# Performance work log

Measured on AMD Instinct MI355X. Metric: run time of the kernel, lower is better.

Reference implementation:

```python
import jax, jax.numpy as jnp
import numpy as np

B, D, H = 4096, 1024, 1024
LN_EPS = 1e-5


def setup_inputs() -> dict:
    key = jax.random.key(0)
    ks = jax.random.split(key, 5)
    return {
        "x": jax.random.normal(ks[0], (B, D), dtype=jnp.float32),
        "prev_h": jax.random.normal(ks[1], (B, H), dtype=jnp.float32),
        "prev_c": jax.random.normal(ks[2], (B, H), dtype=jnp.float32),
        "Wx": jax.random.normal(ks[3], (D, 4 * H), dtype=jnp.float32) * 0.01,
        "Wh": jax.random.normal(ks[4], (H, 4 * H), dtype=jnp.float32) * 0.01,
        "b": jnp.zeros((4 * H,), dtype=jnp.float32),
        "ln_gamma": jnp.ones((4 * H,), dtype=jnp.float32),
        "ln_beta": jnp.zeros((4 * H,), dtype=jnp.float32),
    }


def reference(x, prev_h, prev_c, Wx, Wh, b, ln_gamma, ln_beta):
    # pre-activations: [B, 4H]
    a = x @ Wx + prev_h @ Wh + b
    # LayerNorm over last dim (use_ln=True)
    mu = jnp.mean(a, axis=-1, keepdims=True)
    var = jnp.mean(jnp.square(a - mu), axis=-1, keepdims=True)
    a = (a - mu) * jax.lax.rsqrt(var + LN_EPS) * ln_gamma + ln_beta
    i = jax.nn.sigmoid(a[:, :H])
    f = jax.nn.sigmoid(a[:, H:2 * H])
    o = jax.nn.sigmoid(a[:, 2 * H:3 * H])
    g = jnp.tanh(a[:, 3 * H:])
    next_c = f * prev_c + i * g
    next_h = o * jnp.tanh(next_c)
    # dropout=0.0 -> identity
    return (next_h, next_c)
```

## Files before the change

### kernel.cpp

```cpp
#include <hip/hip_runtime.h>
#include <hip/hip_bf16.h>
#include <stdint.h>

typedef unsigned short u16;
typedef __attribute__((ext_vector_type(8))) short short8;
typedef __attribute__((ext_vector_type(16))) float f32x16;

#define B_DIM 4096
#define D_DIM 1024
#define H_DIM 1024
#define K_DIM 2048
#define N_DIM 4096
#define LN_EPS 1e-5f

__device__ __forceinline__ u16 f2bf(float f) {
    union { float f; uint32_t u; } v; v.f = f;
    uint32_t u = v.u;
    uint32_t r = (u + 0x7FFFu + ((u >> 16) & 1u)) >> 16;
    return (u16)r;
}
__device__ __forceinline__ float bf2f(u16 h) {
    union { uint32_t u; float f; } v; v.u = ((uint32_t)h) << 16;
    return v.f;
}
__device__ __forceinline__ void gld16(const u16* g, u16* l) {
    __builtin_amdgcn_global_load_lds(
        (const __attribute__((address_space(1))) void*)g,
        (__attribute__((address_space(3))) void*)l,
        16, 0, 0);
}
__device__ __forceinline__ float sigm(float x) { return 1.0f / (1.0f + __expf(-x)); }
__device__ __forceinline__ float tanh_fast(float x) { return 1.0f - 2.0f / (__expf(2.0f * x) + 1.0f); }

__global__ __launch_bounds__(256) void prep(const float* __restrict__ x,
                                            const float* __restrict__ h,
                                            const float* __restrict__ Wx,
                                            const float* __restrict__ Wh,
                                            u16* __restrict__ A,
                                            u16* __restrict__ Bt) {
    __shared__ u16 tile[64 * 64];
    const int t = threadIdx.x;
    if (blockIdx.x < 4096) {
        int id = blockIdx.x * 256 + t;
        int row = id >> 8;
        int col = (id & 255) * 8;
        const float* src = (col < D_DIM) ? (x + (size_t)row * D_DIM + col)
                                         : (h + (size_t)row * H_DIM + (col - D_DIM));
        float4 v0 = ((const float4*)src)[0];
        float4 v1 = ((const float4*)src)[1];
        union { u16 us[8]; uint4 u; } p;
        p.us[0] = f2bf(v0.x); p.us[1] = f2bf(v0.y); p.us[2] = f2bf(v0.z); p.us[3] = f2bf(v0.w);
        p.us[4] = f2bf(v1.x); p.us[5] = f2bf(v1.y); p.us[6] = f2bf(v1.z); p.us[7] = f2bf(v1.w);
        *(uint4*)(A + (size_t)id * 8) = p.u;
    } else {
        const int v = blockIdx.x - 4096;
        const int n0 = (v & 63) * 64;
        const int k0 = (v >> 6) * 64;
        const int kl  = t >> 4;
        const int nl4 = (t & 15) * 4;
#pragma unroll
        for (int it = 0; it < 4; ++it) {
            const int klocal = kl + it * 16;
            const int k = k0 + klocal;
            const float* src = (k < D_DIM) ? (Wx + (size_t)k * N_DIM)
                                           : (Wh + (size_t)(k - D_DIM) * N_DIM);
            float4 w = *(const float4*)(src + n0 + nl4);
            union { u16 us[4]; uint2 u; } p;
            p.us[0] = f2bf(w.x); p.us[1] = f2bf(w.y); p.us[2] = f2bf(w.z); p.us[3] = f2bf(w.w);
            const int swz = 8 * ((klocal >> 4) & 3);
            *(uint2*)(tile + klocal * 64 + (nl4 ^ swz)) = p.u;
        }
        __syncthreads();
        const int nl = t >> 2;
        const int kp = (t & 3) * 16;
        const int swz = 8 * (t & 3);
        union { u16 us[16]; uint4 q[2]; } o;
#pragma unroll
        for (int i = 0; i < 16; ++i)
            o.us[i] = tile[(kp + i) * 64 + (nl ^ swz)];
        u16* dst = Bt + (size_t)(n0 + nl) * K_DIM + k0 + kp;
        *(uint4*)dst = o.q[0];
        *(uint4*)(dst + 8) = o.q[1];
    }
}

__global__ __launch_bounds__(256, 1) void gemm_bf16(const u16* __restrict__ A,
                                                    const u16* __restrict__ Bt,
                                                    const float* __restrict__ bias,
                                                    u16* __restrict__ C) {
    __shared__ u16 As[2][16384];
    __shared__ u16 Bs[2][16384];
    const int tid = threadIdx.x;
    const int wave = tid >> 6, lane = tid & 63;
    const int m0 = blockIdx.y * 256;
    const int n0 = blockIdx.x * 256;
    const int wm = (wave & 1) * 128;
    const int wn = (wave >> 1) * 128;

    f32x16 acc[4][4] = {};

    const int perm = ((lane & 3) - (lane >> 3)) & 3;
    const int vofs = (lane >> 2) * K_DIM + perm * 8;
    const int lr = lane & 31, half = lane >> 5;

    for (int it = 0; it < K_DIM / 64 + 1; ++it) {
        if (it < K_DIM / 64) {
            const int kt = it * 64;
            const int buf = it & 1;
#pragma unroll
            for (int q = 0; q < 8; ++q) {
                const int ch = wave * 8 + q;
                const int hp = ch >> 4, c = ch & 15;
                const int so = (c * 16) * K_DIM + kt + hp * 32;
                const int ldso = hp * 8192 + c * 512;
                gld16(A  + (size_t)m0 * K_DIM + so + vofs, &As[buf][ldso]);
                gld16(Bt + (size_t)n0 * K_DIM + so + vofs, &Bs[buf][ldso]);
            }
        }
        if (it == 0) { __syncthreads(); continue; }

        const int cbuf = (it - 1) & 1;
#pragma unroll
        for (int kk = 0; kk < 4; ++kk) {
            const int hp = kk >> 1;
            const int s = (((kk & 1) * 2 + half) + (lr >> 1)) & 3;
            const int ko = hp * 8192 + s * 8;
            short8 af[4], bf[4];
#pragma unroll
            for (int i = 0; i < 4; ++i)
                af[i] = *(const short8*)(&As[cbuf][ko + (wm + i * 32 + lr) * 32]);
#pragma unroll
            for (int j = 0; j < 4; ++j)
                bf[j] = *(const short8*)(&Bs[cbuf][ko + (wn + j * 32 + lr) * 32]);
#pragma unroll
            for (int i = 0; i < 4; ++i)
#pragma unroll
                for (int j = 0; j < 4; ++j)
                    acc[i][j] = __builtin_amdgcn_mfma_f32_32x32x16_bf16(af[i], bf[j], acc[i][j], 0, 0, 0);
        }
        __syncthreads();
    }

#pragma unroll
    for (int i = 0; i < 4; ++i) {
#pragma unroll
        for (int j = 0; j < 4; ++j) {
            const int c = n0 + wn + 32 * j + lr;
            const float bb = bias[c];
#pragma unroll
            for (int reg = 0; reg < 16; ++reg) {
                const int row = m0 + wm + 32 * i + (reg & 3) + 8 * (reg >> 2) + 4 * half;
                C[(size_t)row * N_DIM + c] = f2bf(acc[i][j][reg] + bb);
            }
        }
    }
}

__global__ __launch_bounds__(256) void ln_lstm(const u16* __restrict__ aT,
                                               const float* __restrict__ pc,
                                               const float* __restrict__ gamma,
                                               const float* __restrict__ beta,
                                               float* __restrict__ out) {
    const int row = blockIdx.x;
    const int t = threadIdx.x;
    const u16* ar = aT + (size_t)row * N_DIM;
    const int j0 = t * 4;

    union U2 { uint2 u; u16 us[4]; };
    U2 g4[4];
#pragma unroll
    for (int s = 0; s < 4; ++s) g4[s].u = *(const uint2*)(ar + s * H_DIM + j0);

    float sum = 0.f, ssq = 0.f;
#pragma unroll
    for (int s = 0; s < 4; ++s)
#pragma unroll
        for (int e = 0; e < 4; ++e) { float v = bf2f(g4[s].us[e]); sum += v; ssq += v * v; }

#pragma unroll
    for (int off = 32; off > 0; off >>= 1) {
        sum += __shfl_down(sum, off, 64);
        ssq += __shfl_down(ssq, off, 64);
    }
    __shared__ float red[8];
    if ((t & 63) == 0) { red[t >> 6] = sum; red[4 + (t >> 6)] = ssq; }
    __syncthreads();
    const float ts = red[0] + red[1] + red[2] + red[3];
    const float tq = red[4] + red[5] + red[6] + red[7];
    const float mu = ts * (1.0f / N_DIM);
    const float var = fmaxf(tq * (1.0f / N_DIM) - mu * mu, 0.0f);
    const float rs = rsqrtf(var + LN_EPS);

    float vi[4], vf[4], vo[4], vg[4];
    auto gate = [&](int s, float* v) {
        const int off = s * H_DIM;
        float4 gm = *(const float4*)(gamma + off + j0);
        float4 bt = *(const float4*)(beta + off + j0);
        v[0] = (bf2f(g4[s].us[0]) - mu) * rs * gm.x + bt.x;
        v[1] = (bf2f(g4[s].us[1]) - mu) * rs * gm.y + bt.y;
        v[2] = (bf2f(g4[s].us[2]) - mu) * rs * gm.z + bt.z;
        v[3] = (bf2f(g4[s].us[3]) - mu) * rs * gm.w + bt.w;
    };
    gate(0, vi); gate(1, vf); gate(2, vo); gate(3, vg);

    float4 c4 = *(const float4*)(pc + (size_t)row * H_DIM + j0);
    float cin[4] = {c4.x, c4.y, c4.z, c4.w};
    float nh[4], nc[4];
#pragma unroll
    for (int r = 0; r < 4; ++r) {
        float ig = sigm(vi[r]);
        float fg = sigm(vf[r]);
        float og = sigm(vo[r]);
        float gg = tanh_fast(vg[r]);
        nc[r] = fg * cin[r] + ig * gg;
        nh[r] = og * tanh_fast(nc[r]);
    }
    float4 h4 = {nh[0], nh[1], nh[2], nh[3]};
    float4 c4o = {nc[0], nc[1], nc[2], nc[3]};
    *(float4*)(out + (size_t)row * H_DIM + j0) = h4;
    *(float4*)(out + (size_t)B_DIM * H_DIM + (size_t)row * H_DIM + j0) = c4o;
}

extern "C" void kernel_launch(void* const* d_in, const int* in_sizes, int n_in,
                              void* d_out, int out_size, void* d_ws, size_t ws_size,
                              hipStream_t stream) {
    const float* x  = (const float*)d_in[0];
    const float* ph = (const float*)d_in[1];
    const float* pc = (const float*)d_in[2];
    const float* Wx = (const float*)d_in[3];
    const float* Wh = (const float*)d_in[4];
    const float* b  = (const float*)d_in[5];
    const float* gm = (const float*)d_in[6];
    const float* bt = (const float*)d_in[7];
    float* out = (float*)d_out;

    char* ws = (char*)d_ws;
    u16* Abf = (u16*)ws;
    u16* Btb = (u16*)(ws + (size_t)16 * 1024 * 1024);
    u16* aT  = (u16*)(ws + (size_t)32 * 1024 * 1024);

    prep<<<dim3(4096 + 2048), dim3(256), 0, stream>>>(x, ph, Wx, Wh, Abf, Btb);
    gemm_bf16<<<dim3(16, 16), dim3(256), 0, stream>>>(Abf, Btb, b, aT);
    ln_lstm<<<dim3(4096), dim3(256), 0, stream>>>(aT, pc, gm, bt, out);
}
```

Baseline: 224.2 us.

## Restructure bf16 GEMM into 8-wave half-K-step pipeline with block swizzle

Doubles the GEMM workgroup to 8 waves, each computing a 128x64 sub-tile, and splits each 64-wide K tile into two 32-wide halves. Global-to-LDS loads of upcoming halves are issued between the LDS fragment reads and the MFMA burst, with explicit vmcnt waits, barriers and setprio raised around the MFMAs. A block-index swizzle also remaps tiles to change L2 locality. The aim is better overlap of memory and MFMA work with less register pressure per wave, at the cost of more barriers and hand-tuned wait counts that must match the issued loads exactly.

```diff
diff --git a/kernel.cpp b/kernel.cpp
--- a/kernel.cpp
+++ b/kernel.cpp
@@ -84,7 +84,7 @@
     }
 }
 
-__global__ __launch_bounds__(256, 1) void gemm_bf16(const u16* __restrict__ A,
+__global__ __launch_bounds__(512, 2) void gemm_bf16(const u16* __restrict__ A,
                                                     const u16* __restrict__ Bt,
                                                     const float* __restrict__ bias,
                                                     u16* __restrict__ C) {
@@ -92,59 +92,93 @@
     __shared__ u16 Bs[2][16384];
     const int tid = threadIdx.x;
     const int wave = tid >> 6, lane = tid & 63;
-    const int m0 = blockIdx.y * 256;
-    const int n0 = blockIdx.x * 256;
+
+    const int bid = blockIdx.y * 16 + blockIdx.x;
+    const int swz_bid = (bid & 7) * 32 + (bid >> 3);
+    const int m0 = (swz_bid >> 4) * 256;
+    const int n0 = (swz_bid & 15) * 256;
+
     const int wm = (wave & 1) * 128;
-    const int wn = (wave >> 1) * 128;
-
-    f32x16 acc[4][4] = {};
+    const int wn = (wave >> 1) * 64;
+
+    f32x16 acc[4][2] = {};
 
     const int perm = ((lane & 3) - (lane >> 3)) & 3;
     const int vofs = (lane >> 2) * K_DIM + perm * 8;
     const int lr = lane & 31, half = lane >> 5;
 
-    for (int it = 0; it < K_DIM / 64 + 1; ++it) {
-        if (it < K_DIM / 64) {
-            const int kt = it * 64;
-            const int buf = it & 1;
-#pragma unroll
-            for (int q = 0; q < 8; ++q) {
-                const int ch = wave * 8 + q;
-                const int hp = ch >> 4, c = ch & 15;
-                const int so = (c * 16) * K_DIM + kt + hp * 32;
-                const int ldso = hp * 8192 + c * 512;
-                gld16(A  + (size_t)m0 * K_DIM + so + vofs, &As[buf][ldso]);
-                gld16(Bt + (size_t)n0 * K_DIM + so + vofs, &Bs[buf][ldso]);
-            }
+    const u16* Ab = A  + (size_t)m0 * K_DIM;
+    const u16* Bb = Bt + (size_t)n0 * K_DIM;
+
+    auto stage = [&](int buf, int t, int h) {
+        const int kt = t * 64;
+#pragma unroll
+        for (int q = 0; q < 2; ++q) {
+            const int c = wave * 2 + q;
+            const int so = (c * 16) * K_DIM + kt + h * 32;
+            const int ldso = h * 8192 + c * 512;
+            gld16(Ab + so + vofs, &As[buf][ldso]);
+            gld16(Bb + so + vofs, &Bs[buf][ldso]);
         }
-        if (it == 0) { __syncthreads(); continue; }
-
-        const int cbuf = (it - 1) & 1;
-#pragma unroll
-        for (int kk = 0; kk < 4; ++kk) {
-            const int hp = kk >> 1;
-            const int s = (((kk & 1) * 2 + half) + (lr >> 1)) & 3;
-            const int ko = hp * 8192 + s * 8;
-            short8 af[4], bf[4];
-#pragma unroll
-            for (int i = 0; i < 4; ++i)
-                af[i] = *(const short8*)(&As[cbuf][ko + (wm + i * 32 + lr) * 32]);
-#pragma unroll
-            for (int j = 0; j < 4; ++j)
-                bf[j] = *(const short8*)(&Bs[cbuf][ko + (wn + j * 32 + lr) * 32]);
-#pragma unroll
-            for (int i = 0; i < 4; ++i)
-#pragma unroll
-                for (int j = 0; j < 4; ++j)
-                    acc[i][j] = __builtin_amdgcn_mfma_f32_32x32x16_bf16(af[i], bf[j], acc[i][j], 0, 0, 0);
-        }
-        __syncthreads();
-    }
+    };
+
+#define VMWAIT(n) asm volatile("s_waitcnt vmcnt(" #n ")" ::: "memory")
+
+#define PHASE(BUF, KH, STAGE_STMT, VM)                                               \
+    {                                                                                \
+        short8 af[2][4], bfr[2][2];                                                  \
+        _Pragma("unroll")                                                            \
+        for (int kk2 = 0; kk2 < 2; ++kk2) {                                          \
+            const int s = ((kk2 * 2 + half) + (lr >> 1)) & 3;                        \
+            const int ko = (KH) * 8192 + s * 8;                                      \
+            _Pragma("unroll")                                                        \
+            for (int i = 0; i < 4; ++i)                                              \
+                af[kk2][i] = *(const short8*)(&As[BUF][ko + (wm + i * 32 + lr) * 32]); \
+            _Pragma("unroll")                                                        \
+            for (int j = 0; j < 2; ++j)                                              \
+                bfr[kk2][j] = *(const short8*)(&Bs[BUF][ko + (wn + j * 32 + lr) * 32]); \
+        }                                                                            \
+        STAGE_STMT;                                                                  \
+        asm volatile("s_waitcnt vmcnt(" #VM ")" ::: "memory");                       \
+        __builtin_amdgcn_s_barrier();                                                \
+        __builtin_amdgcn_s_setprio(1);                                               \
+        _Pragma("unroll")                                                            \
+        for (int kk2 = 0; kk2 < 2; ++kk2)                                            \
+            _Pragma("unroll")                                                        \
+            for (int i = 0; i < 4; ++i)                                              \
+                _Pragma("unroll")                                                    \
+                for (int j = 0; j < 2; ++j)                                          \
+                    acc[i][j] = __builtin_amdgcn_mfma_f32_32x32x16_bf16(             \
+                        af[kk2][i], bfr[kk2][j], acc[i][j], 0, 0, 0);                \
+        __builtin_amdgcn_s_setprio(0);                                               \
+        __builtin_amdgcn_s_barrier();                                                \
+    }
+
+    stage(0, 0, 0);
+    stage(0, 0, 1);
+    stage(1, 1, 0);
+    VMWAIT(4);
+    __builtin_amdgcn_s_barrier();
+
+    for (int t2 = 0; t2 < 15; ++t2) {
+        const int t = t2 * 2;
+        PHASE(0, 0, stage(1, t + 1, 1), 8);
+        PHASE(0, 1, stage(0, t + 2, 0), 8);
+        PHASE(1, 0, stage(0, t + 2, 1), 8);
+        PHASE(1, 1, stage(1, t + 3, 0), 8);
+    }
+    PHASE(0, 0, stage(1, 31, 1), 8);
+    PHASE(0, 1, ;, 4);
+    PHASE(1, 0, ;, 0);
+    PHASE(1, 1, ;, 0);
+
+#undef PHASE
+#undef VMWAIT
 
 #pragma unroll
     for (int i = 0; i < 4; ++i) {
 #pragma unroll
-        for (int j = 0; j < 4; ++j) {
+        for (int j = 0; j < 2; ++j) {
             const int c = n0 + wn + 32 * j + lr;
             const float bb = bias[c];
 #pragma unroll
@@ -240,6 +274,6 @@
     u16* aT  = (u16*)(ws + (size_t)32 * 1024 * 1024);
 
     prep<<<dim3(4096 + 2048), dim3(256), 0, stream>>>(x, ph, Wx, Wh, Abf, Btb);
-    gemm_bf16<<<dim3(16, 16), dim3(256), 0, stream>>>(Abf, Btb, b, aT);
+    gemm_bf16<<<dim3(16, 16), dim3(512), 0, stream>>>(Abf, Btb, b, aT);
     ln_lstm<<<dim3(4096), dim3(256), 0, stream>>>(aT, pc, gm, bt, out);
 }
```

Measured after the change: 215.7 us. 1.04x faster.

## Restructure bf16 GEMM into 8-wave phased pipeline with block swizzle

Applied to the files above, without the earlier changes.

The GEMM kernel moves from 4 to 8 waves per block, each wave owning a 128x64 tile. The K loop is split into fine-grained phases that interleave LDS fragment reads, async global-to-LDS staging of half-tiles and MFMA bursts under raised priority. Each phase uses partial vmcnt waits and raw barriers. Block IDs are swizzled to improve L2 reuse of A and B tiles. The aim is to hide global load latency behind MFMA work, at the cost of more complex sync. The prefetch runs past the last K tile and reads beyond the end of each row.

```diff
diff --git a/kernel.cpp b/kernel.cpp
--- a/kernel.cpp
+++ b/kernel.cpp
@@ -84,67 +84,101 @@
     }
 }
 
-__global__ __launch_bounds__(256, 1) void gemm_bf16(const u16* __restrict__ A,
+__global__ __launch_bounds__(512, 2) void gemm_bf16(const u16* __restrict__ A,
                                                     const u16* __restrict__ Bt,
                                                     const float* __restrict__ bias,
                                                     u16* __restrict__ C) {
-    __shared__ u16 As[2][16384];
-    __shared__ u16 Bs[2][16384];
+    __shared__ u16 As[2][2][8192];
+    __shared__ u16 Bs[2][2][8192];
     const int tid = threadIdx.x;
     const int wave = tid >> 6, lane = tid & 63;
-    const int m0 = blockIdx.y * 256;
-    const int n0 = blockIdx.x * 256;
-    const int wm = (wave & 1) * 128;
-    const int wn = (wave >> 1) * 128;
-
-    f32x16 acc[4][4] = {};
-
-    const int perm = ((lane & 3) - (lane >> 3)) & 3;
-    const int vofs = (lane >> 2) * K_DIM + perm * 8;
+
+    const int bid = blockIdx.y * 16 + blockIdx.x;
+    const int swz_bid = (bid & 7) * 32 + (bid >> 3);
+    const int m0 = (swz_bid >> 4) * 256;
+    const int n0 = (swz_bid & 15) * 256;
+
+    const int wr = wave & 1, wc = wave >> 1;
+    const int wm = wr * 128, wn = wc * 64;
     const int lr = lane & 31, half = lane >> 5;
 
-    for (int it = 0; it < K_DIM / 64 + 1; ++it) {
-        if (it < K_DIM / 64) {
-            const int kt = it * 64;
-            const int buf = it & 1;
-#pragma unroll
-            for (int q = 0; q < 8; ++q) {
-                const int ch = wave * 8 + q;
-                const int hp = ch >> 4, c = ch & 15;
-                const int so = (c * 16) * K_DIM + kt + hp * 32;
-                const int ldso = hp * 8192 + c * 512;
-                gld16(A  + (size_t)m0 * K_DIM + so + vofs, &As[buf][ldso]);
-                gld16(Bt + (size_t)n0 * K_DIM + so + vofs, &Bs[buf][ldso]);
-            }
-        }
-        if (it == 0) { __syncthreads(); continue; }
-
-        const int cbuf = (it - 1) & 1;
-#pragma unroll
-        for (int kk = 0; kk < 4; ++kk) {
-            const int hp = kk >> 1;
-            const int s = (((kk & 1) * 2 + half) + (lr >> 1)) & 3;
-            const int ko = hp * 8192 + s * 8;
-            short8 af[4], bf[4];
-#pragma unroll
-            for (int i = 0; i < 4; ++i)
-                af[i] = *(const short8*)(&As[cbuf][ko + (wm + i * 32 + lr) * 32]);
-#pragma unroll
-            for (int j = 0; j < 4; ++j)
-                bf[j] = *(const short8*)(&Bs[cbuf][ko + (wn + j * 32 + lr) * 32]);
-#pragma unroll
-            for (int i = 0; i < 4; ++i)
-#pragma unroll
-                for (int j = 0; j < 4; ++j)
-                    acc[i][j] = __builtin_amdgcn_mfma_f32_32x32x16_bf16(af[i], bf[j], acc[i][j], 0, 0, 0);
-        }
-        __syncthreads();
-    }
+    f32x16 acc[4][2] = {};
+
+    const int srow = wave * 16 + (lane >> 2);
+    const int qsrc = (lane & 3) ^ ((lane >> 3) & 3);
+    const u16* Asrc = A  + (size_t)(m0 + srow) * K_DIM + qsrc * 8;
+    const u16* Bsrc = Bt + (size_t)(n0 + srow) * K_DIM + qsrc * 8;
+    const int ldst = wave * 512;
+
+    auto stageA = [&](int buf, int tt, int ks) {
+        const int ko = tt * 64 + ks * 32;
+        gld16(Asrc + ko,                         &As[buf][ks][ldst]);
+        gld16(Asrc + ko + (size_t)128 * K_DIM,   &As[buf][ks][ldst + 4096]);
+    };
+    auto stageB = [&](int buf, int tt, int ks) {
+        const int ko = tt * 64 + ks * 32;
+        gld16(Bsrc + ko,                         &Bs[buf][ks][ldst]);
+        gld16(Bsrc + ko + (size_t)128 * K_DIM,   &Bs[buf][ks][ldst + 4096]);
+    };
+
+    const int sA = (lr >> 1) & 3;
+    const int aoff = (wm + lr) * 32;
+    const int boff = (wn + lr) * 32;
+
+    short8 af[2][4], bf[2];
+
+#define PHASE(BUF, KS, QJ, READ_A, STAGE_STMT, DO_VM)                                  \
+    {                                                                                  \
+        if (READ_A) {                                                                  \
+            _Pragma("unroll")                                                          \
+            for (int kk = 0; kk < 2; ++kk)                                             \
+                _Pragma("unroll")                                                      \
+                for (int i = 0; i < 4; ++i)                                            \
+                    af[kk][i] = *(const short8*)(                                      \
+                        &As[BUF][KS][aoff + i * 1024 + (((kk * 2 + half) ^ sA) << 3)]);\
+        }                                                                              \
+        _Pragma("unroll")                                                              \
+        for (int kk = 0; kk < 2; ++kk)                                                 \
+            bf[kk] = *(const short8*)(                                                 \
+                &Bs[BUF][KS][boff + (QJ) * 1024 + (((kk * 2 + half) ^ sA) << 3)]);     \
+        STAGE_STMT;                                                                    \
+        __builtin_amdgcn_s_setprio(1);                                                 \
+        _Pragma("unroll")                                                              \
+        for (int kk = 0; kk < 2; ++kk)                                                 \
+            _Pragma("unroll")                                                          \
+            for (int i = 0; i < 4; ++i)                                                \
+                acc[i][QJ] = __builtin_amdgcn_mfma_f32_32x32x16_bf16(                  \
+                    af[kk][i], bf[kk], acc[i][QJ], 0, 0, 0);                           \
+        __builtin_amdgcn_s_setprio(0);                                                 \
+        if (DO_VM) asm volatile("s_waitcnt vmcnt(8)" ::: "memory");                    \
+        __builtin_amdgcn_s_barrier();                                                  \
+        asm volatile("" ::: "memory");                                                 \
+    }
+
+    stageA(0, 0, 0); stageB(0, 0, 0);
+    stageA(0, 0, 1); stageB(0, 0, 1);
+    stageA(1, 1, 0); stageB(1, 1, 0);
+    asm volatile("s_waitcnt vmcnt(0)" ::: "memory");
+    __builtin_amdgcn_s_barrier();
+    asm volatile("" ::: "memory");
+
+    for (int it = 0; it < 16; ++it) {
+        const int t = it * 2;
+        PHASE(0, 0, 0, true,  stageA(1, t + 1, 1), false);
+        PHASE(0, 0, 1, false, stageB(1, t + 1, 1), true );
+        PHASE(0, 1, 1, true,  stageA(0, t + 2, 0), false);
+        PHASE(0, 1, 0, false, stageB(0, t + 2, 0), true );
+        PHASE(1, 0, 0, true,  stageA(0, t + 2, 1), false);
+        PHASE(1, 0, 1, false, stageB(0, t + 2, 1), true );
+        PHASE(1, 1, 1, true,  stageA(1, t + 3, 0), false);
+        PHASE(1, 1, 0, false, stageB(1, t + 3, 0), true );
+    }
+#undef PHASE
 
 #pragma unroll
     for (int i = 0; i < 4; ++i) {
 #pragma unroll
-        for (int j = 0; j < 4; ++j) {
+        for (int j = 0; j < 2; ++j) {
             const int c = n0 + wn + 32 * j + lr;
             const float bb = bias[c];
 #pragma unroll
@@ -240,6 +274,6 @@
     u16* aT  = (u16*)(ws + (size_t)32 * 1024 * 1024);
 
     prep<<<dim3(4096 + 2048), dim3(256), 0, stream>>>(x, ph, Wx, Wh, Abf, Btb);
-    gemm_bf16<<<dim3(16, 16), dim3(256), 0, stream>>>(Abf, Btb, b, aT);
+    gemm_bf16<<<dim3(16, 16), dim3(512), 0, stream>>>(Abf, Btb, b, aT);
     ln_lstm<<<dim3(4096), dim3(256), 0, stream>>>(aT, pc, gm, bt, out);
 }
```

Measured after the change: 214.8 us. -4.2%, faster.
